# Performance work log

Measured on AMD Instinct MI355X. Metric: run time of the kernel, lower is better.

Reference implementation:

```python
import jax, jax.numpy as jnp
import numpy as np

NUM_FEATURES = 1024
NUM_GROUPS = 64
NUM_POS = 3
BATCH = 8192  # rows per view; N = NUM_POS * BATCH


def setup_inputs() -> dict:
    key = jax.random.key(0)
    kx, kp = jax.random.split(key)
    x = jax.random.normal(kx, (NUM_POS * BATCH, NUM_FEATURES), dtype=jnp.float32)
    # one independent column permutation per view (deterministic stand-in for torch.randperm)
    pkeys = jax.random.split(kp, NUM_POS)
    perms = jnp.stack([jax.random.permutation(k, NUM_FEATURES) for k in pkeys]).astype(jnp.int32)
    return {"x": x, "perms": perms}


def _group_whiten(x, perms):
    # x: [N, D] with N = 3*B; perms: [3, D]
    N, D = x.shape
    B = N // NUM_POS
    G = NUM_GROUPS
    d = D // G
    xs = x.reshape(NUM_POS, B, D)                                  # [3, B, D]
    # shuffle feature columns per view: x.t()[perm].t()
    xp = jnp.take_along_axis(xs, perms[:, None, :], axis=2)        # [3, B, D]
    xg = xp.reshape(NUM_POS, B, G, d)                              # [3, B, G, d]
    xc = xg - xg.mean(axis=1, keepdims=True)                       # center over batch
    xt = xc.transpose(0, 2, 1, 3)                                  # [3, G, B, d]
    cov = jnp.einsum('sgbd,sgbe->sgde', xt, xt) / B                # [3, G, d, d]
    S, U = jnp.linalg.eigh(cov)                                    # symmetric eig (symeig)
    # W = U diag(S^-1/2) U^T
    W = jnp.einsum('sgde,sge,sgfe->sgdf', U, jax.lax.rsqrt(S), U)  # [3, G, d, d]
    y = jnp.einsum('sgbd,sgde->sgbe', xt, W)                       # [3, G, B, d]
    # unshuffle: transpose(1,2).flatten(0,1)[argsort(perm)].t()
    yf = y.transpose(0, 1, 3, 2).reshape(NUM_POS, D, B)            # [3, D, B]
    inv = jnp.argsort(perms, axis=1)                               # inverse permutation
    yu = jnp.take_along_axis(yf, inv[:, :, None], axis=1)          # [3, D, B]
    return yu.transpose(0, 2, 1).reshape(N, D)                     # [N, D]


def reference(x, perms):
    return _group_whiten(x, perms)
```

## Files before the change

### kernel.cpp

```cpp
#include <hip/hip_runtime.h>
#include <stdint.h>


constexpr int D_FEAT  = 1024;
constexpr int NGROUP  = 64;
constexpr int GD      = 16;
constexpr int NB      = 8192;
constexpr int NVIEW   = 3;

constexpr int P1      = 256;
constexpr int RPP1    = NB / P1;
constexpr int RPB3    = 32;
constexpr int C3      = 4;
constexpr int PSPLIT  = 8;

constexpr int SXX_FLOATS  = NGROUP * GD * GD;
constexpr int PART_STRIDE = SXX_FLOATS + D_FEAT;
constexpr int ENT         = NVIEW * PART_STRIDE;

constexpr int SXX_OFF = 0;
constexpr int SX_OFF  = NVIEW * SXX_FLOATS;
constexpr int W_OFF   = SX_OFF + NVIEW * D_FEAT;
constexpr int RED_OFF = W_OFF + NVIEW * SXX_FLOATS;

template <int B>
__device__ __forceinline__ float qbc(float x) {
    return __int_as_float(__builtin_amdgcn_mov_dpp(
        __float_as_int(x), B * 0x55 , 0xF, 0xF, true));
}

__global__ __launch_bounds__(256, 3) void k_stats_gather(const float* __restrict__ x,
                                                         const int* __restrict__ perms,
                                                         float* __restrict__ part) {
    const int s   = blockIdx.y;
    const int p   = blockIdx.x;
    const int tid = threadIdx.x;

    int pcolq[4];
#pragma unroll
    for (int jj = 0; jj < 4; ++jj) pcolq[jj] = perms[s * D_FEAT + tid * 4 + jj];

    float acc[GD][4];
#pragma unroll
    for (int i = 0; i < GD; ++i)
#pragma unroll
        for (int jj = 0; jj < 4; ++jj) acc[i][jj] = 0.0f;
    float sacc[4] = {0.0f, 0.0f, 0.0f, 0.0f};

    const float* xbase = x + (size_t)(s * NB + p * RPP1) * D_FEAT;

#define ROW_ACC(Q0, Q1, Q2, Q3)                                                \
    {                                                                          \
        float vq_[4] = {Q0, Q1, Q2, Q3};                                       \
        float v_[GD];                                                          \
        _Pragma("unroll")                                                      \
        for (int jj = 0; jj < 4; ++jj) {                                       \
            v_[0  + jj] = qbc<0>(vq_[jj]);                                     \
            v_[4  + jj] = qbc<1>(vq_[jj]);                                     \
            v_[8  + jj] = qbc<2>(vq_[jj]);                                     \
            v_[12 + jj] = qbc<3>(vq_[jj]);                                     \
        }                                                                      \
        _Pragma("unroll")                                                      \
        for (int jj = 0; jj < 4; ++jj) sacc[jj] += vq_[jj];                    \
        _Pragma("unroll")                                                      \
        for (int i = 0; i < GD; ++i)                                           \
            _Pragma("unroll")                                                  \
            for (int jj = 0; jj < 4; ++jj)                                     \
                acc[i][jj] = fmaf(v_[i], vq_[jj], acc[i][jj]);                 \
    }

    for (int r = 0; r < RPP1; r += 2) {
        const float* ra = xbase + (size_t)r * D_FEAT;
        const float* rb = ra + D_FEAT;
        const float a0 = ra[pcolq[0]], a1 = ra[pcolq[1]],
                    a2 = ra[pcolq[2]], a3 = ra[pcolq[3]];
        const float b0 = rb[pcolq[0]], b1 = rb[pcolq[1]],
                    b2 = rb[pcolq[2]], b3 = rb[pcolq[3]];
        ROW_ACC(a0, a1, a2, a3)
        ROW_ACC(b0, b1, b2, b3)
    }
#undef ROW_ACC

    float* dst = part + (size_t)(s * P1 + p) * PART_STRIDE;
#pragma unroll
    for (int i = 0; i < GD; ++i)
        *(float4*)&dst[i * D_FEAT + tid * 4] =
            make_float4(acc[i][0], acc[i][1], acc[i][2], acc[i][3]);
    *(float4*)&dst[SXX_FLOATS + tid * 4] = make_float4(sacc[0], sacc[1], sacc[2], sacc[3]);
}

__global__ __launch_bounds__(256) void k_reduce1(const float* __restrict__ part,
                                                 float* __restrict__ red) {
    const int f = blockIdx.x * 256 + threadIdx.x;
    if (f >= ENT) return;
    const int s = f / PART_STRIDE, ff = f % PART_STRIDE;
    constexpr int PER = P1 / PSPLIT;
    const float* src = part + ((size_t)s * P1 + blockIdx.y * PER) * PART_STRIDE + ff;
    float sum = 0.0f;
#pragma unroll 8
    for (int p = 0; p < PER; ++p) sum += src[(size_t)p * PART_STRIDE];
    red[(size_t)blockIdx.y * ENT + f] = sum;
}

__global__ __launch_bounds__(256) void k_reduce2(const float* __restrict__ red,
                                                 float* __restrict__ ws) {
    const int f = blockIdx.x * 256 + threadIdx.x;
    if (f >= ENT) return;
    float sum = 0.0f;
#pragma unroll
    for (int pp = 0; pp < PSPLIT; ++pp) sum += red[(size_t)pp * ENT + f];
    const int s = f / PART_STRIDE, rest = f % PART_STRIDE;
    if (rest < SXX_FLOATS) {
        const int i = rest >> 10;
        const int g = (rest & 1023) >> 4;
        const int j = rest & 15;
        ws[SXX_OFF + (size_t)((s * NGROUP + g) * GD + i) * GD + j] = sum;
    } else {
        ws[SX_OFF + s * D_FEAT + (rest - SXX_FLOATS)] = sum;
    }
}

__global__ __launch_bounds__(256) void k_invsqrt(float* __restrict__ ws) {
    __shared__ float Ym[GD][GD];
    __shared__ float Zm[GD][GD];
    __shared__ float Tm[GD][GD];
    const int bx = blockIdx.x;
    const int s = bx / NGROUP, g = bx % NGROUP;
    const int tid = threadIdx.x;
    const int i = tid >> 4, j = tid & 15;
    const float invB = 1.0f / (float)NB;

    const float sxx = ws[SXX_OFF + (size_t)((s * NGROUP + g) * GD + i) * GD + j];
    const float mui = ws[SX_OFF + s * D_FEAT + g * GD + i] * invB;
    const float muj = ws[SX_OFF + s * D_FEAT + g * GD + j] * invB;
    const float a = sxx * invB - mui * muj;

    Ym[i][j] = a;
    __syncthreads();
    float tr = 0.0f;
#pragma unroll
    for (int k = 0; k < GD; ++k) tr += Ym[k][k];
    const float sc = tr * (1.0f / (float)GD);
    const float inv_sc = 1.0f / sc;
    __syncthreads();
    Ym[i][j] = a * inv_sc;
    Zm[i][j] = (i == j) ? 1.0f : 0.0f;
    __syncthreads();

    float zn = (i == j) ? 1.0f : 0.0f;
    for (int it = 0; it < 6; ++it) {
        float t = 0.0f;
#pragma unroll
        for (int k = 0; k < GD; ++k) t += Zm[i][k] * Ym[k][j];
        t = ((i == j) ? 1.5f : 0.0f) - 0.5f * t;
        Tm[i][j] = t;
        __syncthreads();
        float yn = 0.0f;
        zn = 0.0f;
#pragma unroll
        for (int k = 0; k < GD; ++k) {
            yn += Ym[i][k] * Tm[k][j];
            zn += Tm[i][k] * Zm[k][j];
        }
        __syncthreads();
        Ym[i][j] = yn;
        Zm[i][j] = zn;
        __syncthreads();
    }
    ws[W_OFF + (size_t)((s * NGROUP + g) * GD + i) * GD + j] = zn * rsqrtf(sc);
}

__global__ __launch_bounds__(256, 3) void k_apply(const float* __restrict__ x,
                                                  const int* __restrict__ perms,
                                                  const float* __restrict__ ws,
                                                  float* __restrict__ out) {
    __shared__ float bin[2][C3][D_FEAT];
    __shared__ float bout[C3][D_FEAT];
    const int s   = blockIdx.y;
    const int rb  = blockIdx.x;
    const int tid = threadIdx.x;
    const int g   = tid >> 2;
    const int q   = tid & 3;
    const float invB = 1.0f / (float)NB;

    int pcolq[4];
#pragma unroll
    for (int jj = 0; jj < 4; ++jj) pcolq[jj] = perms[s * D_FEAT + tid * 4 + jj];

    const float* Wp = ws + W_OFF + (size_t)(s * NGROUP + g) * GD * GD;
    float w[GD][4];
#pragma unroll
    for (int e = 0; e < GD; ++e) {
        float4 t4 = *(const float4*)&Wp[e * GD + q * 4];
        w[e][0] = t4.x; w[e][1] = t4.y; w[e][2] = t4.z; w[e][3] = t4.w;
    }
    float bias[4] = {0.0f, 0.0f, 0.0f, 0.0f};
#pragma unroll
    for (int e = 0; e < GD; ++e) {
        const float mu = ws[SX_OFF + s * D_FEAT + g * GD + e] * invB;
#pragma unroll
        for (int ii = 0; ii < 4; ++ii) bias[ii] += mu * w[e][ii];
    }

    const float* xbase = x + (size_t)(s * NB + rb * RPB3) * D_FEAT;
    float* obase = out + (size_t)(s * NB + rb * RPB3) * D_FEAT;
    constexpr int NCH = RPB3 / C3;

    float4 rr[C3];
#pragma unroll
    for (int t = 0; t < C3; ++t)
        rr[t] = *(const float4*)&xbase[(size_t)t * D_FEAT + tid * 4];

    for (int k = 0; k < NCH; ++k) {
#pragma unroll
        for (int t = 0; t < C3; ++t)
            *(float4*)&bin[k & 1][t][tid * 4] = rr[t];
        __syncthreads();
        if (k + 1 < NCH) {
            const float* nx = xbase + (size_t)(k + 1) * C3 * D_FEAT;
#pragma unroll
            for (int t = 0; t < C3; ++t)
                rr[t] = *(const float4*)&nx[(size_t)t * D_FEAT + tid * 4];
        }
        const float (*cb)[D_FEAT] = bin[k & 1];
#pragma unroll
        for (int r = 0; r < C3; ++r) {
            float vq[4];
#pragma unroll
            for (int jj = 0; jj < 4; ++jj) vq[jj] = cb[r][pcolq[jj]];
            float v[GD];
#pragma unroll
            for (int jj = 0; jj < 4; ++jj) {
                v[0  + jj] = qbc<0>(vq[jj]);
                v[4  + jj] = qbc<1>(vq[jj]);
                v[8  + jj] = qbc<2>(vq[jj]);
                v[12 + jj] = qbc<3>(vq[jj]);
            }
            float u[4] = {-bias[0], -bias[1], -bias[2], -bias[3]};
#pragma unroll
            for (int e = 0; e < GD; ++e)
#pragma unroll
                for (int ii = 0; ii < 4; ++ii) u[ii] = fmaf(v[e], w[e][ii], u[ii]);
#pragma unroll
            for (int ii = 0; ii < 4; ++ii) bout[r][pcolq[ii]] = u[ii];
        }
        __syncthreads();
        float* ob = obase + (size_t)k * C3 * D_FEAT;
#pragma unroll
        for (int t = 0; t < C3; ++t)
            *(float4*)&ob[(size_t)t * D_FEAT + tid * 4] =
                *(const float4*)&bout[t][tid * 4];
    }
}

extern "C" void kernel_launch(void* const* d_in, const int* in_sizes, int n_in,
                              void* d_out, int out_size, void* d_ws, size_t ws_size,
                              hipStream_t stream) {
    const float* x     = (const float*)d_in[0];
    const int*   perms = (const int*)d_in[1];
    float* out = (float*)d_out;
    float* ws  = (float*)d_ws;

    float* part = out;

    dim3 g1(P1, NVIEW);
    k_stats_gather<<<g1, 256, 0, stream>>>(x, perms, part);

    dim3 gr1((ENT + 255) / 256, PSPLIT);
    k_reduce1<<<gr1, 256, 0, stream>>>(part, ws + RED_OFF);
    k_reduce2<<<(ENT + 255) / 256, 256, 0, stream>>>(ws + RED_OFF, ws);

    k_invsqrt<<<NVIEW * NGROUP, 256, 0, stream>>>(ws);

    dim3 g3(NB / RPB3, NVIEW);
    k_apply<<<g3, 256, 0, stream>>>(x, perms, ws, out);
}
```

Baseline: 102.9 us.

## Split stats-gather rows across two half-blocks with shared-memory reduction

The covariance-statistics kernel now runs 512 threads per block. Each half accumulates half of the block's rows, and the two halves combine their 16x4 accumulators through a shared-memory exchange before writing partials. The row loop is also unrolled to four rows per iteration. The aim is more waves in flight to hide gather-load latency, at the cost of extra syncs and shared-memory traffic and tighter register limits under launch_bounds(512,6).

```diff
diff --git a/kernel.cpp b/kernel.cpp
--- a/kernel.cpp
+++ b/kernel.cpp
@@ -10,6 +10,7 @@
 
 constexpr int P1      = 256;
 constexpr int RPP1    = NB / P1;
+constexpr int HROWS   = RPP1 / 2;
 constexpr int RPB3    = 32;
 constexpr int C3      = 4;
 constexpr int PSPLIT  = 8;
@@ -29,16 +30,19 @@
         __float_as_int(x), B * 0x55 , 0xF, 0xF, true));
 }
 
-__global__ __launch_bounds__(256, 3) void k_stats_gather(const float* __restrict__ x,
+__global__ __launch_bounds__(512, 6) void k_stats_gather(const float* __restrict__ x,
                                                          const int* __restrict__ perms,
                                                          float* __restrict__ part) {
-    const int s   = blockIdx.y;
-    const int p   = blockIdx.x;
-    const int tid = threadIdx.x;
+    __shared__ float red[256][17];
+    const int s    = blockIdx.y;
+    const int p    = blockIdx.x;
+    const int tid  = threadIdx.x;
+    const int lt   = tid & 255;
+    const int half = tid >> 8;
 
     int pcolq[4];
 #pragma unroll
-    for (int jj = 0; jj < 4; ++jj) pcolq[jj] = perms[s * D_FEAT + tid * 4 + jj];
+    for (int jj = 0; jj < 4; ++jj) pcolq[jj] = perms[s * D_FEAT + lt * 4 + jj];
 
     float acc[GD][4];
 #pragma unroll
@@ -47,7 +51,7 @@
         for (int jj = 0; jj < 4; ++jj) acc[i][jj] = 0.0f;
     float sacc[4] = {0.0f, 0.0f, 0.0f, 0.0f};
 
-    const float* xbase = x + (size_t)(s * NB + p * RPP1) * D_FEAT;
+    const float* xbase = x + (size_t)(s * NB + p * RPP1 + half * HROWS) * D_FEAT;
 
 #define ROW_ACC(Q0, Q1, Q2, Q3)                                                \
     {                                                                          \
@@ -69,24 +73,63 @@
                 acc[i][jj] = fmaf(v_[i], vq_[jj], acc[i][jj]);                 \
     }
 
-    for (int r = 0; r < RPP1; r += 2) {
-        const float* ra = xbase + (size_t)r * D_FEAT;
-        const float* rb = ra + D_FEAT;
-        const float a0 = ra[pcolq[0]], a1 = ra[pcolq[1]],
-                    a2 = ra[pcolq[2]], a3 = ra[pcolq[3]];
-        const float b0 = rb[pcolq[0]], b1 = rb[pcolq[1]],
-                    b2 = rb[pcolq[2]], b3 = rb[pcolq[3]];
+    for (int r = 0; r < HROWS; r += 4) {
+        const float* r0 = xbase + (size_t)r * D_FEAT;
+        const float* r1 = r0 + D_FEAT;
+        const float* r2 = r1 + D_FEAT;
+        const float* r3 = r2 + D_FEAT;
+        const float a0 = r0[pcolq[0]], a1 = r0[pcolq[1]],
+                    a2 = r0[pcolq[2]], a3 = r0[pcolq[3]];
+        const float b0 = r1[pcolq[0]], b1 = r1[pcolq[1]],
+                    b2 = r1[pcolq[2]], b3 = r1[pcolq[3]];
+        const float c0 = r2[pcolq[0]], c1 = r2[pcolq[1]],
+                    c2 = r2[pcolq[2]], c3 = r2[pcolq[3]];
+        const float d0 = r3[pcolq[0]], d1 = r3[pcolq[1]],
+                    d2 = r3[pcolq[2]], d3 = r3[pcolq[3]];
         ROW_ACC(a0, a1, a2, a3)
         ROW_ACC(b0, b1, b2, b3)
+        ROW_ACC(c0, c1, c2, c3)
+        ROW_ACC(d0, d1, d2, d3)
     }
 #undef ROW_ACC
 
-    float* dst = part + (size_t)(s * P1 + p) * PART_STRIDE;
-#pragma unroll
-    for (int i = 0; i < GD; ++i)
-        *(float4*)&dst[i * D_FEAT + tid * 4] =
-            make_float4(acc[i][0], acc[i][1], acc[i][2], acc[i][3]);
-    *(float4*)&dst[SXX_FLOATS + tid * 4] = make_float4(sacc[0], sacc[1], sacc[2], sacc[3]);
+#pragma unroll
+    for (int i0 = 0; i0 < GD; i0 += 4) {
+        __syncthreads();
+        if (half) {
+#pragma unroll
+            for (int i = 0; i < 4; ++i)
+#pragma unroll
+                for (int jj = 0; jj < 4; ++jj)
+                    red[lt][i * 4 + jj] = acc[i0 + i][jj];
+        }
+        __syncthreads();
+        if (!half) {
+#pragma unroll
+            for (int i = 0; i < 4; ++i)
+#pragma unroll
+                for (int jj = 0; jj < 4; ++jj)
+                    acc[i0 + i][jj] += red[lt][i * 4 + jj];
+        }
+    }
+    __syncthreads();
+    if (half) {
+#pragma unroll
+        for (int jj = 0; jj < 4; ++jj) red[lt][jj] = sacc[jj];
+    }
+    __syncthreads();
+
+    if (!half) {
+#pragma unroll
+        for (int jj = 0; jj < 4; ++jj) sacc[jj] += red[lt][jj];
+        float* dst = part + (size_t)(s * P1 + p) * PART_STRIDE;
+#pragma unroll
+        for (int i = 0; i < GD; ++i)
+            *(float4*)&dst[i * D_FEAT + lt * 4] =
+                make_float4(acc[i][0], acc[i][1], acc[i][2], acc[i][3]);
+        *(float4*)&dst[SXX_FLOATS + lt * 4] =
+            make_float4(sacc[0], sacc[1], sacc[2], sacc[3]);
+    }
 }
 
 __global__ __launch_bounds__(256) void k_reduce1(const float* __restrict__ part,
@@ -264,7 +307,7 @@
     float* part = out;
 
     dim3 g1(P1, NVIEW);
-    k_stats_gather<<<g1, 256, 0, stream>>>(x, perms, part);
+    k_stats_gather<<<g1, 512, 0, stream>>>(x, perms, part);
 
     dim3 gr1((ENT + 255) / 256, PSPLIT);
     k_reduce1<<<gr1, 256, 0, stream>>>(part, ws + RED_OFF);
```

Result: slower. 181.0 us (+75.9%).

## Store per-block covariance partials as packed bf16 and double stats parallelism

Applied to the files above, without the earlier changes.

The stats kernel now writes its per-block second-moment and sum partials as packed bf16 pairs, which halves the traffic of the partial buffer, and the first reduce unpacks them into fp32 sums. The number of stats blocks is doubled to 512 with 16 rows each, the inner loop is unrolled to four rows, and the reduce split is raised to 16. Rounding partial sums to bf16 before the reduction costs covariance precision, which may hurt eigenvalue accuracy for the whitening. More blocks also mean more partials to write and reduce.

```diff
diff --git a/kernel.cpp b/kernel.cpp
--- a/kernel.cpp
+++ b/kernel.cpp
@@ -8,15 +8,18 @@
 constexpr int NB      = 8192;
 constexpr int NVIEW   = 3;
 
-constexpr int P1      = 256;
+constexpr int P1      = 512;
 constexpr int RPP1    = NB / P1;
 constexpr int RPB3    = 32;
 constexpr int C3      = 4;
-constexpr int PSPLIT  = 8;
+constexpr int PSPLIT  = 16;
+constexpr int PER     = P1 / PSPLIT;
 
 constexpr int SXX_FLOATS  = NGROUP * GD * GD;
 constexpr int PART_STRIDE = SXX_FLOATS + D_FEAT;
+constexpr int PSTRIDE_U32 = PART_STRIDE / 2;
 constexpr int ENT         = NVIEW * PART_STRIDE;
+constexpr int ENT_DW      = NVIEW * PSTRIDE_U32;
 
 constexpr int SXX_OFF = 0;
 constexpr int SX_OFF  = NVIEW * SXX_FLOATS;
@@ -29,9 +32,16 @@
         __float_as_int(x), B * 0x55 , 0xF, 0xF, true));
 }
 
+__device__ __forceinline__ uint32_t pkbf2(float a, float b) {
+    uint32_t ua = __float_as_uint(a), ub = __float_as_uint(b);
+    ua += 0x7FFFu + ((ua >> 16) & 1u);
+    ub += 0x7FFFu + ((ub >> 16) & 1u);
+    return (ua >> 16) | (ub & 0xFFFF0000u);
+}
+
 __global__ __launch_bounds__(256, 3) void k_stats_gather(const float* __restrict__ x,
                                                          const int* __restrict__ perms,
-                                                         float* __restrict__ part) {
+                                                         uint32_t* __restrict__ part) {
     const int s   = blockIdx.y;
     const int p   = blockIdx.x;
     const int tid = threadIdx.x;
@@ -69,37 +79,53 @@
                 acc[i][jj] = fmaf(v_[i], vq_[jj], acc[i][jj]);                 \
     }
 
-    for (int r = 0; r < RPP1; r += 2) {
-        const float* ra = xbase + (size_t)r * D_FEAT;
-        const float* rb = ra + D_FEAT;
-        const float a0 = ra[pcolq[0]], a1 = ra[pcolq[1]],
-                    a2 = ra[pcolq[2]], a3 = ra[pcolq[3]];
-        const float b0 = rb[pcolq[0]], b1 = rb[pcolq[1]],
-                    b2 = rb[pcolq[2]], b3 = rb[pcolq[3]];
+    for (int r = 0; r < RPP1; r += 4) {
+        const float* r0 = xbase + (size_t)r * D_FEAT;
+        const float* r1 = r0 + D_FEAT;
+        const float* r2 = r1 + D_FEAT;
+        const float* r3 = r2 + D_FEAT;
+        const float a0 = r0[pcolq[0]], a1 = r0[pcolq[1]],
+                    a2 = r0[pcolq[2]], a3 = r0[pcolq[3]];
+        const float b0 = r1[pcolq[0]], b1 = r1[pcolq[1]],
+                    b2 = r1[pcolq[2]], b3 = r1[pcolq[3]];
+        const float c0 = r2[pcolq[0]], c1 = r2[pcolq[1]],
+                    c2 = r2[pcolq[2]], c3 = r2[pcolq[3]];
+        const float d0 = r3[pcolq[0]], d1 = r3[pcolq[1]],
+                    d2 = r3[pcolq[2]], d3 = r3[pcolq[3]];
         ROW_ACC(a0, a1, a2, a3)
         ROW_ACC(b0, b1, b2, b3)
+        ROW_ACC(c0, c1, c2, c3)
+        ROW_ACC(d0, d1, d2, d3)
     }
 #undef ROW_ACC
 
-    float* dst = part + (size_t)(s * P1 + p) * PART_STRIDE;
-#pragma unroll
-    for (int i = 0; i < GD; ++i)
-        *(float4*)&dst[i * D_FEAT + tid * 4] =
-            make_float4(acc[i][0], acc[i][1], acc[i][2], acc[i][3]);
-    *(float4*)&dst[SXX_FLOATS + tid * 4] = make_float4(sacc[0], sacc[1], sacc[2], sacc[3]);
-}
-
-__global__ __launch_bounds__(256) void k_reduce1(const float* __restrict__ part,
+    uint32_t* dst = part + (size_t)(s * P1 + p) * PSTRIDE_U32;
+#pragma unroll
+    for (int i = 0; i < GD; ++i) {
+        dst[i * 512 + tid * 2 + 0] = pkbf2(acc[i][0], acc[i][1]);
+        dst[i * 512 + tid * 2 + 1] = pkbf2(acc[i][2], acc[i][3]);
+    }
+    dst[8192 + tid * 2 + 0] = pkbf2(sacc[0], sacc[1]);
+    dst[8192 + tid * 2 + 1] = pkbf2(sacc[2], sacc[3]);
+}
+
+__global__ __launch_bounds__(256) void k_reduce1(const uint32_t* __restrict__ part,
                                                  float* __restrict__ red) {
-    const int f = blockIdx.x * 256 + threadIdx.x;
-    if (f >= ENT) return;
-    const int s = f / PART_STRIDE, ff = f % PART_STRIDE;
-    constexpr int PER = P1 / PSPLIT;
-    const float* src = part + ((size_t)s * P1 + blockIdx.y * PER) * PART_STRIDE + ff;
-    float sum = 0.0f;
+    const int fd = blockIdx.x * 256 + threadIdx.x;
+    if (fd >= ENT_DW) return;
+    const int s = fd / PSTRIDE_U32, ffd = fd % PSTRIDE_U32;
+    const uint32_t* src =
+        part + ((size_t)s * P1 + blockIdx.y * PER) * PSTRIDE_U32 + ffd;
+    float s0 = 0.0f, s1 = 0.0f;
 #pragma unroll 8
-    for (int p = 0; p < PER; ++p) sum += src[(size_t)p * PART_STRIDE];
-    red[(size_t)blockIdx.y * ENT + f] = sum;
+    for (int p = 0; p < PER; ++p) {
+        const uint32_t u = src[(size_t)p * PSTRIDE_U32];
+        s0 += __uint_as_float(u << 16);
+        s1 += __uint_as_float(u & 0xFFFF0000u);
+    }
+    float* r = red + (size_t)blockIdx.y * ENT + s * PART_STRIDE + ffd * 2;
+    r[0] = s0;
+    r[1] = s1;
 }
 
 __global__ __launch_bounds__(256) void k_reduce2(const float* __restrict__ red,
@@ -261,12 +287,12 @@
     float* out = (float*)d_out;
     float* ws  = (float*)d_ws;
 
-    float* part = out;
+    uint32_t* part = (uint32_t*)out;
 
     dim3 g1(P1, NVIEW);
     k_stats_gather<<<g1, 256, 0, stream>>>(x, perms, part);
 
-    dim3 gr1((ENT + 255) / 256, PSPLIT);
+    dim3 gr1((ENT_DW + 255) / 256, PSPLIT);
     k_reduce1<<<gr1, 256, 0, stream>>>(part, ws + RED_OFF);
     k_reduce2<<<(ENT + 255) / 256, 256, 0, stream>>>(ws + RED_OFF, ws);
 
```

New measurement: 104.6 us. Within noise of the previous version (+1.7%).
